# Optimization experiments

Measured on AMD Instinct MI355X. Metric: run time of the kernel, lower is better.

## Reference

```python
import jax, jax.numpy as jnp
import numpy as np

N, D, H, O, E = 50000, 128, 256, 128, 800000


def setup_inputs() -> dict:
    key = jax.random.key(0)
    ks = jax.random.split(key, 8)
    x = jax.random.normal(ks[0], (N, D), dtype=jnp.float32)
    edge_index = jax.random.randint(ks[1], (2, E), 0, N, dtype=jnp.int64)
    s = lambda k, shp: jax.random.normal(k, shp, dtype=jnp.float32) / np.sqrt(shp[0])
    return {
        "x": x,
        "edge_index": edge_index,
        "W1_l": s(ks[2], (D, H)),
        "W1_r": s(ks[3], (D, H)),
        "b1": jnp.zeros((H,), jnp.float32),
        "W2_l": s(ks[4], (H, O)),
        "W2_r": s(ks[5], (H, O)),
        "b2": jnp.zeros((O,), jnp.float32),
    }


def _sage_conv(x, src, dst, W_l, W_r, b, n_nodes):
    # mean aggregation of source messages into destination nodes
    agg = jax.ops.segment_sum(x[src], dst, num_segments=n_nodes)  # [N, F]
    cnt = jax.ops.segment_sum(jnp.ones(src.shape[0], x.dtype), dst,
                              num_segments=n_nodes)               # [N]
    agg = agg / jnp.maximum(cnt, 1.0)[:, None]
    # lin_l(agg) + lin_r(x); lin_l carries the bias (PyG SAGEConv default)
    return agg @ W_l + b + x @ W_r


def reference(x, edge_index, W1_l, W1_r, b1, W2_l, W2_r, b2):
    src, dst = edge_index[0], edge_index[1]
    h = jax.nn.relu(_sage_conv(x, src, dst, W1_l, W1_r, b1, N))
    out = _sage_conv(h, src, dst, W2_l, W2_r, b2, N)
    return out
```

## Files before the change

### kernel.cpp

```cpp
#include <hip/hip_runtime.h>


#define CAP 64
#define NB 98
#define BSH 9
#define BCAP 9216
#define CHUNK 2048

typedef __attribute__((ext_vector_type(8))) short short8;
typedef __attribute__((ext_vector_type(8))) unsigned short ushort8;
typedef __attribute__((ext_vector_type(4))) float f32x4;

__device__ __forceinline__ unsigned short f2bf(float f) {
  unsigned u = __builtin_bit_cast(unsigned, f);
  u += 0x7fff + ((u >> 16) & 1);
  return (unsigned short)(u >> 16);
}
__device__ __forceinline__ float bf2f(unsigned v) {
  return __builtin_bit_cast(float, v << 16);
}

__global__ __launch_bounds__(256) void prep_kernel(
    const float* __restrict__ x, unsigned short* __restrict__ xb,
    const float* __restrict__ W1l, const float* __restrict__ W1r,
    const float* __restrict__ W2l, const float* __restrict__ W2r,
    unsigned short* __restrict__ Wt1, unsigned short* __restrict__ Wt2,
    int* __restrict__ bcursor, unsigned short* __restrict__ hw, int n8, int N) {
  const int b = blockIdx.x;
  const int t = threadIdx.x;
  if (b == 0) {
    if (t < 128) bcursor[t] = 0;
    if (t < 64) {
      reinterpret_cast<unsigned*>(xb + (size_t)N * 128)[t] = 0u;
      reinterpret_cast<unsigned*>(hw + (size_t)N * 128)[t] = 0u;
    }
  }
  if (b < 256) {
    int idx = b * 256 + t;
    int ch = idx >> 8, k = idx & 255;
    Wt1[idx] = f2bf((k < 128) ? W1l[k * 256 + ch] : W1r[(k - 128) * 256 + ch]);
    Wt2[idx] = f2bf((ch < 128) ? W2l[k * 128 + ch] : W2r[k * 128 + (ch - 128)]);
  } else {
    int i = (b - 256) * 256 + t;
    if (i < n8) {
      const float4* p = reinterpret_cast<const float4*>(x) + (size_t)i * 2;
      float4 a = p[0], bb = p[1];
      union { unsigned short u[8]; int4 v; } r;
      r.u[0]=f2bf(a.x); r.u[1]=f2bf(a.y); r.u[2]=f2bf(a.z); r.u[3]=f2bf(a.w);
      r.u[4]=f2bf(bb.x); r.u[5]=f2bf(bb.y); r.u[6]=f2bf(bb.z); r.u[7]=f2bf(bb.w);
      reinterpret_cast<int4*>(xb)[i] = r.v;
    }
  }
}

__global__ __launch_bounds__(256) void bucket_kernel(
    const int* __restrict__ src, const int* __restrict__ dst,
    int* __restrict__ bcursor, unsigned* __restrict__ buckets, int E) {
  __shared__ unsigned pack[CHUNK];
  __shared__ unsigned char binarr[CHUNK];
  __shared__ unsigned sorted[CHUNK];
  __shared__ unsigned char sbin[CHUNK];
  __shared__ int hist[NB];
  __shared__ int scn[NB + 1];
  __shared__ int gbase[NB];
  const int t = threadIdx.x;
  const int e0 = blockIdx.x * CHUNK;
  const int n = min(CHUNK, E - e0);

  for (int i = t; i < NB; i += 256) hist[i] = 0;
  __syncthreads();
  for (int i = t; i < n; i += 256) {
    int s = src[e0 + i];
    int d = dst[e0 + i];
    int b = d >> BSH;
    pack[i] = ((unsigned)(d & 511) << 16) | (unsigned)s;
    binarr[i] = (unsigned char)b;
    atomicAdd(&hist[b], 1);
  }
  __syncthreads();
  if (t == 0) {
    int a = 0;
    for (int b = 0; b < NB; ++b) { scn[b] = a; a += hist[b]; }
    scn[NB] = a;
  }
  __syncthreads();
  if (t < NB) { gbase[t] = atomicAdd(&bcursor[t], hist[t]); hist[t] = 0; }
  __syncthreads();
  for (int i = t; i < n; i += 256) {
    int b = binarr[i];
    int pos = scn[b] + atomicAdd(&hist[b], 1);
    sorted[pos] = pack[i];
    sbin[pos] = (unsigned char)b;
  }
  __syncthreads();
  for (int i = t; i < n; i += 256) {
    int b = sbin[i];
    int off = gbase[b] + (i - scn[b]);
    if (off < BCAP) buckets[(size_t)b * BCAP + off] = sorted[i];
  }
}

__global__ __launch_bounds__(256) void csr_kernel(
    const int* __restrict__ bcursor, const unsigned* __restrict__ buckets,
    unsigned short* __restrict__ elist, int* __restrict__ deg, int N) {
  __shared__ unsigned short csr[128 * CAP];
  __shared__ int cur[128];
  const int t = threadIdx.x;
  const int b = blockIdx.x >> 2;
  const int q = blockIdx.x & 3;
  if (t < 128) cur[t] = 0;
  __syncthreads();
  const int cnt = min(bcursor[b], BCAP);
  const unsigned* bp = buckets + (size_t)b * BCAP;
  for (int i = t; i < cnt; i += 256) {
    unsigned p = bp[i];
    int lo = p >> 16;
    if ((lo >> 7) == q) {
      int r = lo & 127;
      int pos = atomicAdd(&cur[r], 1);
      if (pos < CAP) csr[r * CAP + pos] = (unsigned short)(p & 0xffffu);
    }
  }
  __syncthreads();
  if (t < 128) {
    int d = min(cur[t], CAP);
    int dgc = (d + 7) & ~7;
    if (dgc < 8) dgc = 8;
    if (dgc > CAP) dgc = CAP;
    for (int p = d; p < dgc; ++p) csr[t * CAP + p] = (unsigned short)N;
  }
  __syncthreads();
  const int node0 = (b << BSH) + (q << 7);
  const int nn = min(128, N - node0);
  if (nn <= 0) return;
  if (t < nn) deg[node0 + t] = min(cur[t], CAP);
  int4* dst4 = reinterpret_cast<int4*>(elist + (size_t)node0 * CAP);
  const int4* src4 = reinterpret_cast<const int4*>(csr);
  for (int i = t; i < nn * 8; i += 256) dst4[i] = src4[i];
}

#define GLD(P, EV) \
  P##0 = f[(size_t)(EV)[0] * 64 + lane]; P##1 = f[(size_t)(EV)[1] * 64 + lane]; \
  P##2 = f[(size_t)(EV)[2] * 64 + lane]; P##3 = f[(size_t)(EV)[3] * 64 + lane]; \
  P##4 = f[(size_t)(EV)[4] * 64 + lane]; P##5 = f[(size_t)(EV)[5] * 64 + lane]; \
  P##6 = f[(size_t)(EV)[6] * 64 + lane]; P##7 = f[(size_t)(EV)[7] * 64 + lane];
#define ACC(P) \
  s0x += bf2f(P##0 & 0xffffu); s0y += bf2f(P##0 >> 16); \
  s1x += bf2f(P##1 & 0xffffu); s1y += bf2f(P##1 >> 16); \
  s2x += bf2f(P##2 & 0xffffu); s2y += bf2f(P##2 >> 16); \
  s3x += bf2f(P##3 & 0xffffu); s3y += bf2f(P##3 >> 16); \
  s0x += bf2f(P##4 & 0xffffu); s0y += bf2f(P##4 >> 16); \
  s1x += bf2f(P##5 & 0xffffu); s1y += bf2f(P##5 >> 16); \
  s2x += bf2f(P##6 & 0xffffu); s2y += bf2f(P##6 >> 16); \
  s3x += bf2f(P##7 & 0xffffu); s3y += bf2f(P##7 >> 16);

template<int MODE>
__global__ __launch_bounds__(256) void aggregate_kernel(
    const unsigned short* __restrict__ feat, const int* __restrict__ deg_,
    const unsigned short* __restrict__ elist, const unsigned short* __restrict__ hr,
    const float* __restrict__ bias, void* __restrict__ outp, int N) {
  const int node = (blockIdx.x * blockDim.x + threadIdx.x) >> 6;
  const int lane = threadIdx.x & 63;
  if (node >= N) return;
  const int deg = deg_[node];
  int dgc = (deg + 7) & ~7; if (dgc < 8) dgc = 8;
  const unsigned* f = reinterpret_cast<const unsigned*>(feat);
  const int4* el4 = reinterpret_cast<const int4*>(elist + (size_t)node * CAP);
  int4 p0 = el4[0], p1 = el4[1], p2 = el4[2], p3 = el4[3],
       p4 = el4[4], p5 = el4[5], p6 = el4[6], p7 = el4[7];
  ushort8 c0 = __builtin_bit_cast(ushort8, p0), c1 = __builtin_bit_cast(ushort8, p1),
          c2 = __builtin_bit_cast(ushort8, p2), c3 = __builtin_bit_cast(ushort8, p3),
          c4 = __builtin_bit_cast(ushort8, p4), c5 = __builtin_bit_cast(ushort8, p5),
          c6 = __builtin_bit_cast(ushort8, p6), c7 = __builtin_bit_cast(ushort8, p7);
  float s0x=0.f,s0y=0.f,s1x=0.f,s1y=0.f,s2x=0.f,s2y=0.f,s3x=0.f,s3y=0.f;
  unsigned a0,a1,a2,a3,a4,a5,a6,a7, b0,b1,b2,b3,b4,b5,b6,b7;
  GLD(a, c0);
  if (dgc > 8)  { GLD(b, c1); }
  ACC(a);
  if (dgc > 16) { GLD(a, c2); }
  if (dgc > 8)  { ACC(b); }
  if (dgc > 24) { GLD(b, c3); }
  if (dgc > 16) { ACC(a); }
  if (dgc > 32) { GLD(a, c4); }
  if (dgc > 24) { ACC(b); }
  if (dgc > 40) { GLD(b, c5); }
  if (dgc > 32) { ACC(a); }
  if (dgc > 48) { GLD(a, c6); }
  if (dgc > 40) { ACC(b); }
  if (dgc > 56) { GLD(b, c7); }
  if (dgc > 48) { ACC(a); }
  if (dgc > 56) { ACC(b); }
  float inv = 1.0f / (float)max(deg, 1);
  float rx = (s0x + s1x + s2x + s3x) * inv;
  float ry = (s0y + s1y + s2y + s3y) * inv;
  if constexpr (MODE == 0) {
    unsigned r = (unsigned)f2bf(rx) | ((unsigned)f2bf(ry) << 16);
    reinterpret_cast<unsigned*>(outp)[(size_t)node * 64 + lane] = r;
  } else {
    unsigned res = reinterpret_cast<const unsigned*>(hr)[(size_t)node * 64 + lane];
    float2 bb = reinterpret_cast<const float2*>(bias)[lane];
    float2 o;
    o.x = rx + bf2f(res & 0xffffu) + bb.x;
    o.y = ry + bf2f(res >> 16) + bb.y;
    reinterpret_cast<float2*>(outp)[(size_t)node * 64 + lane] = o;
  }
}

__global__ __launch_bounds__(256, 2) void fused_gemm_kernel(
    const unsigned short* __restrict__ aggb, const unsigned short* __restrict__ xb,
    const unsigned short* __restrict__ Wt1, const unsigned short* __restrict__ Wt2,
    const float* __restrict__ b1,
    unsigned short* __restrict__ hw, unsigned short* __restrict__ hr, int N) {
  __shared__ int4 As4[512];
  __shared__ int4 Bs4[2048];
  __shared__ int4 hL4[2048];
  char* As = reinterpret_cast<char*>(As4);
  char* Bs = reinterpret_cast<char*>(Bs4);
  char* hL = reinterpret_cast<char*>(hL4);
  const int t = threadIdx.x;
  const int lane = t & 63;
  const int hi = lane >> 4;
  const int lo = lane & 15;
  const int wv = t >> 6;
  const int n0 = blockIdx.x * 64;
  const int cw = wv * 64;

  f32x4 acc[4][4];
  #pragma unroll
  for (int m = 0; m < 4; ++m)
    #pragma unroll
    for (int n = 0; n < 4; ++n)
      acc[m][n] = (f32x4){0.f, 0.f, 0.f, 0.f};

  for (int k0 = 0; k0 < 256; k0 += 64) {
    const unsigned short* Asrc = (k0 < 128) ? aggb : xb;
    const int kk0 = k0 & 127;
    #pragma unroll
    for (int i = 0; i < 2; ++i) {
      int chunk = i * 256 + t;
      int r = chunk >> 3, c16 = chunk & 7;
      int row = n0 + r; if (row >= N) row = N - 1;
      int4 v = *reinterpret_cast<const int4*>(Asrc + (size_t)row * 128 + kk0 + c16 * 8);
      *reinterpret_cast<int4*>(As + r * 128 + ((c16 * 16) ^ ((r & 7) << 4))) = v;
    }
    #pragma unroll
    for (int i = 0; i < 8; ++i) {
      int chunk = i * 256 + t;
      int cc = chunk >> 3, c16 = chunk & 7;
      int4 v = *reinterpret_cast<const int4*>(Wt1 + (size_t)cc * 256 + k0 + c16 * 8);
      *reinterpret_cast<int4*>(Bs + cc * 128 + ((c16 * 16) ^ ((cc & 7) << 4))) = v;
    }
    __syncthreads();
    #pragma unroll
    for (int kk = 0; kk < 64; kk += 32) {
      const int kb = (kk + hi * 8) * 2;
      short8 af[4], bfr[4];
      #pragma unroll
      for (int m = 0; m < 4; ++m) {
        int r = m * 16 + lo;
        af[m] = *reinterpret_cast<const short8*>(As + r * 128 + (kb ^ ((r & 7) << 4)));
      }
      #pragma unroll
      for (int n = 0; n < 4; ++n) {
        int c = cw + n * 16 + lo;
        bfr[n] = *reinterpret_cast<const short8*>(Bs + c * 128 + (kb ^ ((c & 7) << 4)));
      }
      #pragma unroll
      for (int m = 0; m < 4; ++m)
        #pragma unroll
        for (int n = 0; n < 4; ++n)
          acc[m][n] = __builtin_amdgcn_mfma_f32_16x16x32_bf16(af[m], bfr[n], acc[m][n], 0, 0, 0);
    }
    __syncthreads();
  }

  #pragma unroll
  for (int n = 0; n < 4; ++n) {
    const int col = cw + n * 16 + lo;
    const float bv = b1[col];
    const int seg = col >> 6;
    const int wb = (col & 63) * 2;
    #pragma unroll
    for (int m = 0; m < 4; ++m) {
      f32x4 v = acc[m][n];
      #pragma unroll
      for (int j = 0; j < 4; ++j) {
        int row = m * 16 + hi * 4 + j;
        float f = fmaxf(v[j] + bv, 0.0f);
        *reinterpret_cast<unsigned short*>(
            hL + row * 512 + seg * 128 + (wb ^ ((row & 7) << 4))) = f2bf(f);
      }
    }
  }
  __syncthreads();

  f32x4 acc2[4][4];
  #pragma unroll
  for (int m = 0; m < 4; ++m)
    #pragma unroll
    for (int n = 0; n < 4; ++n)
      acc2[m][n] = (f32x4){0.f, 0.f, 0.f, 0.f};

  for (int k0 = 0; k0 < 256; k0 += 64) {
    #pragma unroll
    for (int i = 0; i < 8; ++i) {
      int chunk = i * 256 + t;
      int cc = chunk >> 3, c16 = chunk & 7;
      int4 v = *reinterpret_cast<const int4*>(Wt2 + (size_t)cc * 256 + k0 + c16 * 8);
      *reinterpret_cast<int4*>(Bs + cc * 128 + ((c16 * 16) ^ ((cc & 7) << 4))) = v;
    }
    __syncthreads();
    #pragma unroll
    for (int kk = 0; kk < 64; kk += 32) {
      const int kb = (kk + hi * 8) * 2;
      short8 af[4], bfr[4];
      #pragma unroll
      for (int m = 0; m < 4; ++m) {
        int r = m * 16 + lo;
        af[m] = *reinterpret_cast<const short8*>(hL + r * 512 + k0 * 2 + (kb ^ ((r & 7) << 4)));
      }
      #pragma unroll
      for (int n = 0; n < 4; ++n) {
        int c = cw + n * 16 + lo;
        bfr[n] = *reinterpret_cast<const short8*>(Bs + c * 128 + (kb ^ ((c & 7) << 4)));
      }
      #pragma unroll
      for (int m = 0; m < 4; ++m)
        #pragma unroll
        for (int n = 0; n < 4; ++n)
          acc2[m][n] = __builtin_amdgcn_mfma_f32_16x16x32_bf16(af[m], bfr[n], acc2[m][n], 0, 0, 0);
    }
    __syncthreads();
  }

  unsigned short* dstp = (cw < 128) ? hw : hr;
  const int cbase = cw & 127;
  #pragma unroll
  for (int n = 0; n < 4; ++n) {
    const int col = cbase + n * 16 + lo;
    #pragma unroll
    for (int m = 0; m < 4; ++m) {
      f32x4 v = acc2[m][n];
      #pragma unroll
      for (int j = 0; j < 4; ++j) {
        int row = n0 + m * 16 + hi * 4 + j;
        if (row < N) dstp[(size_t)row * 128 + col] = f2bf(v[j]);
      }
    }
  }
}

extern "C" void kernel_launch(void* const* d_in, const int* in_sizes, int n_in,
                              void* d_out, int out_size, void* d_ws, size_t ws_size,
                              hipStream_t stream) {
  const float* x   = (const float*)d_in[0];
  const int*   ei  = (const int*)d_in[1];
  const float* W1l = (const float*)d_in[2];
  const float* W1r = (const float*)d_in[3];
  const float* b1  = (const float*)d_in[4];
  const float* W2l = (const float*)d_in[5];
  const float* W2r = (const float*)d_in[6];
  const float* b2  = (const float*)d_in[7];
  float* out = (float*)d_out;

  const int N = in_sizes[0] / 128;
  const int E = in_sizes[1] / 2;
  const int* src = ei;
  const int* dst = ei + E;

  int* iws = (int*)d_ws;
  int* bcursor = iws;
  unsigned* buckets = (unsigned*)(iws + 128);
  int* deg = (int*)(buckets + (size_t)NB * BCAP);
  unsigned short* elist = (unsigned short*)(deg + ((N + 64) & ~63));
  unsigned short* xb   = elist + (size_t)N * CAP;
  unsigned short* aggb = xb + (size_t)(N + 8) * 128;
  unsigned short* hw   = aggb + (size_t)N * 128;
  unsigned short* hr   = hw + (size_t)(N + 8) * 128;
  unsigned short* Wt1  = hr + (size_t)N * 128;
  unsigned short* Wt2  = Wt1 + 65536;

  const int n8 = N * 128 / 8;
  prep_kernel<<<256 + (n8 + 255) / 256, 256, 0, stream>>>(
      x, xb, W1l, W1r, W2l, W2r, Wt1, Wt2, bcursor, hw, n8, N);

  bucket_kernel<<<(E + CHUNK - 1) / CHUNK, 256, 0, stream>>>(src, dst, bcursor, buckets, E);
  csr_kernel<<<NB * 4, 256, 0, stream>>>(bcursor, buckets, elist, deg, N);

  const int aggBlocks = (N * 64 + 255) / 256;
  const int MB = (N + 63) / 64;

  aggregate_kernel<0><<<aggBlocks, 256, 0, stream>>>(xb, deg, elist, nullptr, nullptr, (void*)aggb, N);
  fused_gemm_kernel<<<MB, 256, 0, stream>>>(aggb, xb, Wt1, Wt2, b1, hw, hr, N);
  aggregate_kernel<1><<<aggBlocks, 256, 0, stream>>>(hw, deg, elist, hr, b2, (void*)out, N);
}
```

Baseline: 127.9 us.

## Load weights straight from global into registers and share one LDS tile

The fused GEMM kernel now stages the full 64x256 A tile (agg and x concatenated) into shared memory once. Both GEMMs read their weight fragments directly from global memory (L2-cached) into registers instead of cooperatively staging them through LDS. The layer-1 output reuses the same LDS buffer. This removes most __syncthreads and cuts LDS use from about 72KB to 32KB, which may raise occupancy. The cost is uncoalesced, per-wave redundant global weight loads that rely on cache hits.

```diff
diff --git a/kernel.cpp b/kernel.cpp
--- a/kernel.cpp
+++ b/kernel.cpp
@@ -211,12 +211,8 @@
     const unsigned short* __restrict__ Wt1, const unsigned short* __restrict__ Wt2,
     const float* __restrict__ b1,
     unsigned short* __restrict__ hw, unsigned short* __restrict__ hr, int N) {
-  __shared__ int4 As4[512];
-  __shared__ int4 Bs4[2048];
-  __shared__ int4 hL4[2048];
-  char* As = reinterpret_cast<char*>(As4);
-  char* Bs = reinterpret_cast<char*>(Bs4);
-  char* hL = reinterpret_cast<char*>(hL4);
+  __shared__ int4 AH4[2048];
+  char* AH = reinterpret_cast<char*>(AH4);
   const int t = threadIdx.x;
   const int lane = t & 63;
   const int hi = lane >> 4;
@@ -225,6 +221,18 @@
   const int n0 = blockIdx.x * 64;
   const int cw = wv * 64;
 
+  #pragma unroll
+  for (int i = 0; i < 8; ++i) {
+    int chunk = i * 256 + t;
+    int r = chunk >> 5, c16 = chunk & 31;
+    int row = n0 + r; if (row >= N) row = N - 1;
+    const unsigned short* srcp = (c16 < 16) ? (aggb + (size_t)row * 128 + c16 * 8)
+                                            : (xb + (size_t)row * 128 + (c16 - 16) * 8);
+    int4 v = *reinterpret_cast<const int4*>(srcp);
+    *reinterpret_cast<int4*>(AH + r * 512 + ((c16 * 16) ^ ((r & 7) << 4))) = v;
+  }
+  __syncthreads();
+
   f32x4 acc[4][4];
   #pragma unroll
   for (int m = 0; m < 4; ++m)
@@ -232,54 +240,32 @@
     for (int n = 0; n < 4; ++n)
       acc[m][n] = (f32x4){0.f, 0.f, 0.f, 0.f};
 
-  for (int k0 = 0; k0 < 256; k0 += 64) {
-    const unsigned short* Asrc = (k0 < 128) ? aggb : xb;
-    const int kk0 = k0 & 127;
-    #pragma unroll
-    for (int i = 0; i < 2; ++i) {
-      int chunk = i * 256 + t;
-      int r = chunk >> 3, c16 = chunk & 7;
-      int row = n0 + r; if (row >= N) row = N - 1;
-      int4 v = *reinterpret_cast<const int4*>(Asrc + (size_t)row * 128 + kk0 + c16 * 8);
-      *reinterpret_cast<int4*>(As + r * 128 + ((c16 * 16) ^ ((r & 7) << 4))) = v;
-    }
-    #pragma unroll
-    for (int i = 0; i < 8; ++i) {
-      int chunk = i * 256 + t;
-      int cc = chunk >> 3, c16 = chunk & 7;
-      int4 v = *reinterpret_cast<const int4*>(Wt1 + (size_t)cc * 256 + k0 + c16 * 8);
-      *reinterpret_cast<int4*>(Bs + cc * 128 + ((c16 * 16) ^ ((cc & 7) << 4))) = v;
-    }
-    __syncthreads();
-    #pragma unroll
-    for (int kk = 0; kk < 64; kk += 32) {
-      const int kb = (kk + hi * 8) * 2;
-      short8 af[4], bfr[4];
+  #pragma unroll
+  for (int ks = 0; ks < 8; ++ks) {
+    short8 af[4], bfr[4];
+    #pragma unroll
+    for (int n = 0; n < 4; ++n) {
+      int c = cw + n * 16 + lo;
+      bfr[n] = *reinterpret_cast<const short8*>(Wt1 + (size_t)c * 256 + ks * 32 + hi * 8);
+    }
+    const int kb = (ks * 32 + hi * 8) * 2;
+    #pragma unroll
+    for (int m = 0; m < 4; ++m) {
+      int r = m * 16 + lo;
+      af[m] = *reinterpret_cast<const short8*>(AH + r * 512 + (kb ^ ((r & 7) << 4)));
+    }
+    #pragma unroll
+    for (int m = 0; m < 4; ++m)
       #pragma unroll
-      for (int m = 0; m < 4; ++m) {
-        int r = m * 16 + lo;
-        af[m] = *reinterpret_cast<const short8*>(As + r * 128 + (kb ^ ((r & 7) << 4)));
-      }
-      #pragma unroll
-      for (int n = 0; n < 4; ++n) {
-        int c = cw + n * 16 + lo;
-        bfr[n] = *reinterpret_cast<const short8*>(Bs + c * 128 + (kb ^ ((c & 7) << 4)));
-      }
-      #pragma unroll
-      for (int m = 0; m < 4; ++m)
-        #pragma unroll
-        for (int n = 0; n < 4; ++n)
-          acc[m][n] = __builtin_amdgcn_mfma_f32_16x16x32_bf16(af[m], bfr[n], acc[m][n], 0, 0, 0);
-    }
-    __syncthreads();
-  }
+      for (int n = 0; n < 4; ++n)
+        acc[m][n] = __builtin_amdgcn_mfma_f32_16x16x32_bf16(af[m], bfr[n], acc[m][n], 0, 0, 0);
+  }
+  __syncthreads();
 
   #pragma unroll
   for (int n = 0; n < 4; ++n) {
     const int col = cw + n * 16 + lo;
     const float bv = b1[col];
-    const int seg = col >> 6;
-    const int wb = (col & 63) * 2;
     #pragma unroll
     for (int m = 0; m < 4; ++m) {
       f32x4 v = acc[m][n];
@@ -288,7 +274,7 @@
         int row = m * 16 + hi * 4 + j;
         float f = fmaxf(v[j] + bv, 0.0f);
         *reinterpret_cast<unsigned short*>(
-            hL + row * 512 + seg * 128 + (wb ^ ((row & 7) << 4))) = f2bf(f);
+            AH + row * 512 + ((col * 2) ^ ((row & 7) << 4))) = f2bf(f);
       }
     }
   }
@@ -301,36 +287,25 @@
     for (int n = 0; n < 4; ++n)
       acc2[m][n] = (f32x4){0.f, 0.f, 0.f, 0.f};
 
-  for (int k0 = 0; k0 < 256; k0 += 64) {
-    #pragma unroll
-    for (int i = 0; i < 8; ++i) {
-      int chunk = i * 256 + t;
-      int cc = chunk >> 3, c16 = chunk & 7;
-      int4 v = *reinterpret_cast<const int4*>(Wt2 + (size_t)cc * 256 + k0 + c16 * 8);
-      *reinterpret_cast<int4*>(Bs + cc * 128 + ((c16 * 16) ^ ((cc & 7) << 4))) = v;
-    }
-    __syncthreads();
-    #pragma unroll
-    for (int kk = 0; kk < 64; kk += 32) {
-      const int kb = (kk + hi * 8) * 2;
-      short8 af[4], bfr[4];
+  #pragma unroll
+  for (int ks = 0; ks < 8; ++ks) {
+    short8 af[4], bfr[4];
+    #pragma unroll
+    for (int n = 0; n < 4; ++n) {
+      int c = cw + n * 16 + lo;
+      bfr[n] = *reinterpret_cast<const short8*>(Wt2 + (size_t)c * 256 + ks * 32 + hi * 8);
+    }
+    const int kb = (ks * 32 + hi * 8) * 2;
+    #pragma unroll
+    for (int m = 0; m < 4; ++m) {
+      int r = m * 16 + lo;
+      af[m] = *reinterpret_cast<const short8*>(AH + r * 512 + (kb ^ ((r & 7) << 4)));
+    }
+    #pragma unroll
+    for (int m = 0; m < 4; ++m)
       #pragma unroll
-      for (int m = 0; m < 4; ++m) {
-        int r = m * 16 + lo;
-        af[m] = *reinterpret_cast<const short8*>(hL + r * 512 + k0 * 2 + (kb ^ ((r & 7) << 4)));
-      }
-      #pragma unroll
-      for (int n = 0; n < 4; ++n) {
-        int c = cw + n * 16 + lo;
-        bfr[n] = *reinterpret_cast<const short8*>(Bs + c * 128 + (kb ^ ((c & 7) << 4)));
-      }
-      #pragma unroll
-      for (int m = 0; m < 4; ++m)
-        #pragma unroll
-        for (int n = 0; n < 4; ++n)
-          acc2[m][n] = __builtin_amdgcn_mfma_f32_16x16x32_bf16(af[m], bfr[n], acc2[m][n], 0, 0, 0);
-    }
-    __syncthreads();
+      for (int n = 0; n < 4; ++n)
+        acc2[m][n] = __builtin_amdgcn_mfma_f32_16x16x32_bf16(af[m], bfr[n], acc2[m][n], 0, 0, 0);
   }
 
   unsigned short* dstp = (cw < 128) ? hw : hr;
```

Result: slower. 140.9 us (+10.1%).
